# Kernel optimization log

Measured on AMD Instinct MI355X. Metric: run time of the kernel, lower is better.

The kernel has to match this reference:

```python
import jax, jax.numpy as jnp
import numpy as np

B, F, T = 256, 513, 512   # batch, x_dim, seq_len
Z, H, DX, ZG, DZX = 16, 128, 256, 32, 128

def _lin(key, out_d, in_d):
    k1, k2 = jax.random.split(key)
    s = 1.0 / np.sqrt(in_d)
    W = jax.random.uniform(k1, (out_d, in_d), minval=-s, maxval=s, dtype=jnp.float32)
    b = jax.random.uniform(k2, (out_d,), minval=-s, maxval=s, dtype=jnp.float32)
    return W, b

def setup_inputs() -> dict:
    key = jax.random.key(0)
    ks = jax.random.split(key, 20)
    d = {}
    d['x'] = jax.random.normal(ks[0], (B, F, T), dtype=jnp.float32)
    d['eps'] = jax.random.normal(ks[1], (T, B, Z), dtype=jnp.float32)  # reparam noise per step
    # mlp_x_gx: Linear(513,256)+tanh
    d['W_xg'], d['b_xg'] = _lin(ks[2], DX, F)
    # LSTM(256,128), torch gate order i,f,g,o
    s = 1.0 / np.sqrt(H)
    k1, k2, k3, k4 = jax.random.split(ks[3], 4)
    d['W_ih'] = jax.random.uniform(k1, (4 * H, DX), minval=-s, maxval=s, dtype=jnp.float32)
    d['W_hh'] = jax.random.uniform(k2, (4 * H, H), minval=-s, maxval=s, dtype=jnp.float32)
    d['b_ih'] = jax.random.uniform(k3, (4 * H,), minval=-s, maxval=s, dtype=jnp.float32)
    d['b_hh'] = jax.random.uniform(k4, (4 * H,), minval=-s, maxval=s, dtype=jnp.float32)
    # mlp_ztm1_g: Linear(16,32)+tanh, Linear(32,128)+tanh
    d['W_zg0'], d['b_zg0'] = _lin(ks[4], ZG, Z)
    d['W_zg1'], d['b_zg1'] = _lin(ks[5], H, ZG)
    # mlp_g_z = Identity (dense_g_z=[0]); inf heads Linear(128,16)
    d['W_im'], d['b_im'] = _lin(ks[6], Z, H)
    d['W_il'], d['b_il'] = _lin(ks[7], Z, H)
    # gating unit: Linear(16,16)+ReLU, Linear(16,16)+Sigmoid
    d['W_gate0'], d['b_gate0'] = _lin(ks[8], Z, Z)
    d['W_gate1'], d['b_gate1'] = _lin(ks[9], Z, Z)
    # proposed mean: Linear(16,16)+ReLU, Linear(16,16)+Sigmoid
    d['W_prop0'], d['b_prop0'] = _lin(ks[10], Z, Z)
    d['W_prop1'], d['b_prop1'] = _lin(ks[11], Z, Z)
    # prior_mean Linear(16,16); prior_logvar ReLU->Linear(16,16)->Softplus
    d['W_pm'], d['b_pm'] = _lin(ks[12], Z, Z)
    d['W_pl'], d['b_pl'] = _lin(ks[13], Z, Z)
    # mlp_z_x: Linear(16,128)+tanh, Linear(128,128)+tanh; gen_logvar Linear(128,513)
    d['W_zx0'], d['b_zx0'] = _lin(ks[14], DZX, Z)
    d['W_zx1'], d['b_zx1'] = _lin(ks[15], DZX, DZX)
    d['W_gy'], d['b_gy'] = _lin(ks[16], F, DZX)
    return d

def reference(x, eps, W_xg, b_xg, W_ih, W_hh, b_ih, b_hh, W_zg0, b_zg0, W_zg1, b_zg1,
              W_im, b_im, W_il, b_il, W_gate0, b_gate0, W_gate1, b_gate1,
              W_prop0, b_prop0, W_prop1, b_prop1, W_pm, b_pm, W_pl, b_pl,
              W_zx0, b_zx0, W_zx1, b_zx1, W_gy, b_gy):
    xs = jnp.transpose(x, (2, 0, 1))                 # [T,B,F]
    xg = jnp.tanh(xs @ W_xg.T + b_xg)                # [T,B,DX]
    bsz = xs.shape[1]
    Hd = W_hh.shape[1]

    def lstm_step(carry, xt):
        h, c = carry
        gates = xt @ W_ih.T + b_ih + h @ W_hh.T + b_hh
        i, f, g, o = jnp.split(gates, 4, axis=-1)
        c = jax.nn.sigmoid(f) * c + jax.nn.sigmoid(i) * jnp.tanh(g)
        h = jax.nn.sigmoid(o) * jnp.tanh(c)
        return (h, c), h

    h0 = jnp.zeros((bsz, Hd), xg.dtype)
    # module runs LSTM on flipped sequence, then flips output back
    _, g_rev = jax.lax.scan(lstm_step, (h0, h0), xg[::-1])
    g = g_rev[::-1]                                   # [T,B,H]

    def inf_step(z_t, inp):
        g_rnn, e = inp
        hz = jnp.tanh(z_t @ W_zg0.T + b_zg0)
        hz = jnp.tanh(hz @ W_zg1.T + b_zg1)
        g_t = (hz + g_rnn) * 0.5                      # mlp_g_z is Identity
        zm = g_t @ W_im.T + b_im
        zl = g_t @ W_il.T + b_il
        z_new = zm + e * jnp.exp(0.5 * zl)            # reparameterization
        return z_new, (z_new, zm, zl)

    z0 = jnp.zeros((bsz, W_im.shape[0]), xg.dtype)
    _, (z, z_mean, z_logvar) = jax.lax.scan(inf_step, z0, (g, eps))

    # generation_z (gated) -- stored as attributes in the torch module
    z_tm1 = jnp.concatenate([z0[None], z[:-1]], axis=0)
    prop = jax.nn.sigmoid(jax.nn.relu(z_tm1 @ W_prop0.T + b_prop0) @ W_prop1.T + b_prop1)
    gate = jax.nn.sigmoid(jax.nn.relu(z_tm1 @ W_gate0.T + b_gate0) @ W_gate1.T + b_gate1)
    z_mean_p = (1.0 - gate) * (z_tm1 @ W_pm.T + b_pm) + gate * prop
    z_logvar_p = jnp.log(jax.nn.softplus(jax.nn.relu(prop) @ W_pl.T + b_pl))

    # generation_x
    hy = jnp.tanh(z @ W_zx0.T + b_zx0)
    hy = jnp.tanh(hy @ W_zx1.T + b_zx1)
    y = jnp.exp(hy @ W_gy.T + b_gy)                   # [T,B,F]
    return jnp.transpose(y, (1, 2, 0))                # [B,F,T] (forward returns self.y)
```

## Files before the change

kernel.cpp:

```cpp
#include <hip/hip_runtime.h>
#include <cstdint>

#define T_DIM 512
#define B_DIM 256
#define F_DIM 513
#define DX    256
#define H_DIM 128
#define G4    512
#define Z_DIM 16
#define ZG_D  32
#define DZX_D 128
#define M_ROWS (B_DIM * T_DIM)

__device__ __forceinline__ float fast_tanh(float x) {
    return 1.0f - 2.0f / (__expf(2.0f * x) + 1.0f);
}
__device__ __forceinline__ float fast_sig(float x) {
    return 1.0f / (1.0f + __expf(-x));
}

__global__ void bias_comb_kernel(const float* __restrict__ a,
                                 const float* __restrict__ b,
                                 float* __restrict__ c) {
    int i = threadIdx.x;
    if (i < G4) c[i] = a[i] + b[i];
}

template<int ACT, int AMODE, int CMODE, bool GUARD>
__global__ __launch_bounds__(256, 3) void gemm_kernel(
    const float* __restrict__ A, const float* __restrict__ W,
    const float* __restrict__ bias, float* __restrict__ C,
    int M, int N, int K)
{
    __shared__ float As[16][136];
    __shared__ float Bs[16][136];
    const int tid = threadIdx.x;
    const int m0 = blockIdx.y * 128;
    const int n0 = blockIdx.x * 128;
    const int tm = tid >> 4;
    const int tn = tid & 15;
    float acc[8][8] = {};
    const int kTiles = (K + 15) >> 4;
    for (int kt = 0; kt < kTiles; ++kt) {
        const int k0 = kt << 4;
        if (AMODE == 0) {
            const int m  = tid >> 1;
            const int kh = tid & 1;
            const float* ap = &A[(size_t)(m0 + m) * K + k0 + kh * 8];
            const float4 v0 = *(const float4*)(ap);
            const float4 v1 = *(const float4*)(ap + 4);
            As[kh * 8 + 0][m] = v0.x; As[kh * 8 + 1][m] = v0.y;
            As[kh * 8 + 2][m] = v0.z; As[kh * 8 + 3][m] = v0.w;
            As[kh * 8 + 4][m] = v1.x; As[kh * 8 + 5][m] = v1.y;
            As[kh * 8 + 6][m] = v1.z; As[kh * 8 + 7][m] = v1.w;
        } else {
            const int m  = tid & 127;
            const int kh = tid >> 7;
            const int mg = m0 + m;
            const int bb = mg >> 9;
            const int tt = mg & 511;
            const size_t base = (size_t)bb * (F_DIM * T_DIM) + tt;
            #pragma unroll
            for (int j = 0; j < 8; ++j) {
                const int k = k0 + kh * 8 + j;
                As[kh * 8 + j][m] = (k < K) ? A[base + (size_t)k * T_DIM] : 0.0f;
            }
        }
        {
            const int n  = tid >> 1;
            const int kh = tid & 1;
            const int ng = n0 + n;
            if (!GUARD) {
                const float* wp = &W[(size_t)ng * K + k0 + kh * 8];
                const float4 v0 = *(const float4*)(wp);
                const float4 v1 = *(const float4*)(wp + 4);
                Bs[kh * 8 + 0][n] = v0.x; Bs[kh * 8 + 1][n] = v0.y;
                Bs[kh * 8 + 2][n] = v0.z; Bs[kh * 8 + 3][n] = v0.w;
                Bs[kh * 8 + 4][n] = v1.x; Bs[kh * 8 + 5][n] = v1.y;
                Bs[kh * 8 + 6][n] = v1.z; Bs[kh * 8 + 7][n] = v1.w;
            } else {
                #pragma unroll
                for (int j = 0; j < 8; ++j) {
                    const int k = k0 + kh * 8 + j;
                    float v = 0.0f;
                    if (ng < N && k < K) v = W[(size_t)ng * K + k];
                    Bs[kh * 8 + j][n] = v;
                }
            }
        }
        __syncthreads();
        #pragma unroll
        for (int kk = 0; kk < 16; ++kk) {
            const float4 a0 = *(const float4*)&As[kk][tm * 4];
            const float4 a1 = *(const float4*)&As[kk][tm * 4 + 64];
            const float4 b0 = *(const float4*)&Bs[kk][tn * 4];
            const float4 b1 = *(const float4*)&Bs[kk][tn * 4 + 64];
            const float a[8] = { a0.x, a0.y, a0.z, a0.w, a1.x, a1.y, a1.z, a1.w };
            const float b[8] = { b0.x, b0.y, b0.z, b0.w, b1.x, b1.y, b1.z, b1.w };
            #pragma unroll
            for (int i = 0; i < 8; ++i)
                #pragma unroll
                for (int j = 0; j < 8; ++j)
                    acc[i][j] += a[i] * b[j];
        }
        __syncthreads();
    }
    #pragma unroll
    for (int i = 0; i < 8; ++i) {
        const int m = m0 + ((i < 4) ? (tm * 4 + i) : (tm * 4 + 64 + (i - 4)));
        if (CMODE == 0) {
            float r0[4], r1[4];
            #pragma unroll
            for (int j = 0; j < 4; ++j) {
                const int na = n0 + tn * 4 + j;
                float v = acc[i][j] + bias[na];
                if (ACT == 1) v = fast_tanh(v);
                else if (ACT == 2) v = __expf(v);
                r0[j] = v;
                const int nb = n0 + 64 + tn * 4 + j;
                float u = acc[i][j + 4] + bias[nb];
                if (ACT == 1) u = fast_tanh(u);
                else if (ACT == 2) u = __expf(u);
                r1[j] = u;
            }
            *(float4*)&C[(size_t)m * N + n0 + tn * 4]      = make_float4(r0[0], r0[1], r0[2], r0[3]);
            *(float4*)&C[(size_t)m * N + n0 + 64 + tn * 4] = make_float4(r1[0], r1[1], r1[2], r1[3]);
        } else {
            const int bb = m >> 9;
            const int tt = m & 511;
            #pragma unroll
            for (int j = 0; j < 8; ++j) {
                const int n = n0 + ((j < 4) ? (tn * 4 + j) : (64 + tn * 4 + (j - 4)));
                if (n < N) {
                    float v = acc[i][j] + bias[n];
                    if (ACT == 1) v = fast_tanh(v);
                    else if (ACT == 2) v = __expf(v);
                    C[(size_t)bb * (F_DIM * T_DIM) + (size_t)n * T_DIM + tt] = v;
                }
            }
        }
    }
}

#define PIN4(v) asm volatile("" : "+v"((v).x), "+v"((v).y), "+v"((v).z), "+v"((v).w))

__global__ __launch_bounds__(512, 2) void lstm_kernel(
    const float* __restrict__ gin,
    const float* __restrict__ W_hh,
    float* __restrict__ g_out)
{
    __shared__ float hbuf[2][128];
    const int tid  = threadIdx.x;
    const int b    = blockIdx.x;
    const int lane = tid & 63;
    const int w    = tid >> 6;
    const int j    = w * 16 + (lane & 15);
    const int kq   = lane >> 4;

    float4 wi[8], wf[8], wg[8], wo[8];
    {
        const float4* w4 = (const float4*)W_hh;
        const int cb = kq * 8;
        #pragma unroll
        for (int q = 0; q < 8; ++q) {
            wi[q] = w4[(size_t)(j      ) * 32 + cb + q];
            wf[q] = w4[(size_t)(j + 128) * 32 + cb + q];
            wg[q] = w4[(size_t)(j + 256) * 32 + cb + q];
            wo[q] = w4[(size_t)(j + 384) * 32 + cb + q];
        }
        #pragma unroll
        for (int q = 0; q < 8; ++q) { PIN4(wi[q]); PIN4(wf[q]); PIN4(wg[q]); PIN4(wo[q]); }
    }
    if (tid < 128) { hbuf[0][tid] = 0.f; hbuf[1][tid] = 0.f; }
    float c = 0.0f;
    __syncthreads();

    const float* ginb = gin + (size_t)b * T_DIM * G4;
    float gi = ginb[(size_t)(T_DIM - 1) * G4 + j];
    float gf = ginb[(size_t)(T_DIM - 1) * G4 + j + 128];
    float gg = ginb[(size_t)(T_DIM - 1) * G4 + j + 256];
    float go = ginb[(size_t)(T_DIM - 1) * G4 + j + 384];

    int buf = 0;
    for (int t = T_DIM - 1; t >= 0; --t) {
        float ngi = 0.f, ngf = 0.f, ngg = 0.f, ngo = 0.f;
        if (t > 0) {
            const size_t base = (size_t)(t - 1) * G4;
            ngi = ginb[base + j];
            ngf = ginb[base + j + 128];
            ngg = ginb[base + j + 256];
            ngo = ginb[base + j + 384];
        }
        float si = 0.f, sf = 0.f, sg = 0.f, so = 0.f;
        {
            const float4* h4 = (const float4*)&hbuf[buf][kq * 32];
            #pragma unroll
            for (int q = 0; q < 8; ++q) {
                const float4 hv = h4[q];
                si += wi[q].x * hv.x + wi[q].y * hv.y + wi[q].z * hv.z + wi[q].w * hv.w;
                sf += wf[q].x * hv.x + wf[q].y * hv.y + wf[q].z * hv.z + wf[q].w * hv.w;
                sg += wg[q].x * hv.x + wg[q].y * hv.y + wg[q].z * hv.z + wg[q].w * hv.w;
                so += wo[q].x * hv.x + wo[q].y * hv.y + wo[q].z * hv.z + wo[q].w * hv.w;
            }
        }
        si += __shfl_xor(si, 16, 64); si += __shfl_xor(si, 32, 64);
        sf += __shfl_xor(sf, 16, 64); sf += __shfl_xor(sf, 32, 64);
        sg += __shfl_xor(sg, 16, 64); sg += __shfl_xor(sg, 32, 64);
        so += __shfl_xor(so, 16, 64); so += __shfl_xor(so, 32, 64);
        si += gi; sf += gf; sg += gg; so += go;
        c = fast_sig(sf) * c + fast_sig(si) * fast_tanh(sg);
        const float h = fast_sig(so) * fast_tanh(c);
        buf ^= 1;
        if (kq == 0) {
            hbuf[buf][j] = h;
            g_out[((size_t)b * T_DIM + t) * H_DIM + j] = h;
        }
        __syncthreads();
        gi = ngi; gf = ngf; gg = ngg; go = ngo;
        #pragma unroll
        for (int q = 0; q < 8; ++q) { PIN4(wi[q]); PIN4(wf[q]); PIN4(wg[q]); PIN4(wo[q]); }
    }
}

__global__ __launch_bounds__(64, 1) void infer_kernel(
    const float* __restrict__ g,
    const float* __restrict__ eps,
    const float* __restrict__ W_zg0, const float* __restrict__ b_zg0,
    const float* __restrict__ W_zg1, const float* __restrict__ b_zg1,
    const float* __restrict__ W_im,  const float* __restrict__ b_im,
    const float* __restrict__ W_il,  const float* __restrict__ b_il,
    float* __restrict__ z_out)
{
    __shared__ float zbuf[16];
    __shared__ float hzbuf[32];
    __shared__ float h2buf[128];
    const int l = threadIdx.x;
    const int b = blockIdx.x;

    const int r0 = l & 31;
    float4 wz0[4];
    #pragma unroll
    for (int q = 0; q < 4; ++q) wz0[q] = ((const float4*)W_zg0)[r0 * 4 + q];
    const float bz0 = b_zg0[r0];
    float4 w1a[8], w1b[8];
    #pragma unroll
    for (int q = 0; q < 8; ++q) {
        w1a[q] = ((const float4*)W_zg1)[l * 8 + q];
        w1b[q] = ((const float4*)W_zg1)[(l + 64) * 8 + q];
    }
    const float bz1a = b_zg1[l], bz1b = b_zg1[l + 64];
    const int o = l & 31;
    const int half = l >> 5;
    const float* w3p = (o < 16) ? (W_im + o * 128) : (W_il + (o - 16) * 128);
    float4 w3[16];
    #pragma unroll
    for (int q = 0; q < 16; ++q) w3[q] = ((const float4*)(w3p + half * 64))[q];
    const float b3 = (o < 16) ? b_im[o] : b_il[o - 16];

    if (l < 16) zbuf[l] = 0.0f;
    __syncthreads();

    const float* gb = g + (size_t)b * T_DIM * 128;
    float ngl0 = gb[l];
    float ngl1 = gb[64 + l];
    float neps = (l < 16) ? eps[(size_t)b * 16 + l] : 0.0f;
    for (int t = 0; t < T_DIM; ++t) {
        const float gl0 = ngl0, gl1 = ngl1, epsv = neps;
        if (t + 1 < T_DIM) {
            ngl0 = gb[(size_t)(t + 1) * 128 + l];
            ngl1 = gb[(size_t)(t + 1) * 128 + 64 + l];
            neps = (l < 16) ? eps[((size_t)(t + 1) * B_DIM + b) * 16 + l] : 0.0f;
        }
        float s1 = bz0;
        {
            const float4* z4 = (const float4*)zbuf;
            #pragma unroll
            for (int q = 0; q < 4; ++q) {
                const float4 zv = z4[q];
                s1 += wz0[q].x * zv.x + wz0[q].y * zv.y + wz0[q].z * zv.z + wz0[q].w * zv.w;
            }
        }
        const float hz = fast_tanh(s1);
        __syncthreads();
        if (l < 32) hzbuf[l] = hz;
        __syncthreads();
        float s2a = bz1a, s2b = bz1b;
        {
            const float4* hz4 = (const float4*)hzbuf;
            #pragma unroll
            for (int q = 0; q < 8; ++q) {
                const float4 hv = hz4[q];
                s2a += w1a[q].x * hv.x + w1a[q].y * hv.y + w1a[q].z * hv.z + w1a[q].w * hv.w;
                s2b += w1b[q].x * hv.x + w1b[q].y * hv.y + w1b[q].z * hv.z + w1b[q].w * hv.w;
            }
        }
        const float gt0 = 0.5f * (fast_tanh(s2a) + gl0);
        const float gt1 = 0.5f * (fast_tanh(s2b) + gl1);
        __syncthreads();
        h2buf[l]      = gt0;
        h2buf[l + 64] = gt1;
        __syncthreads();
        float s3 = 0.0f;
        {
            const float4* h24 = (const float4*)(h2buf + half * 64);
            #pragma unroll
            for (int q = 0; q < 16; ++q) {
                const float4 hv = h24[q];
                s3 += w3[q].x * hv.x + w3[q].y * hv.y + w3[q].z * hv.z + w3[q].w * hv.w;
            }
        }
        const float full = s3 + __shfl_xor(s3, 32, 64);
        const float val = full + b3;
        const float other = __shfl_xor(val, 16, 64);
        const float znew = val + epsv * __expf(0.5f * other);
        __syncthreads();
        if (l < 16) {
            zbuf[l] = znew;
            z_out[((size_t)b * T_DIM + t) * 16 + l] = znew;
        }
        __syncthreads();
    }
}

extern "C" void kernel_launch(void* const* d_in, const int* in_sizes, int n_in,
                              void* d_out, int out_size, void* d_ws, size_t ws_size,
                              hipStream_t stream)
{
    const float* x     = (const float*)d_in[0];
    const float* eps   = (const float*)d_in[1];
    const float* W_xg  = (const float*)d_in[2];
    const float* b_xg  = (const float*)d_in[3];
    const float* W_ih  = (const float*)d_in[4];
    const float* W_hh  = (const float*)d_in[5];
    const float* b_ih  = (const float*)d_in[6];
    const float* b_hh  = (const float*)d_in[7];
    const float* W_zg0 = (const float*)d_in[8];
    const float* b_zg0 = (const float*)d_in[9];
    const float* W_zg1 = (const float*)d_in[10];
    const float* b_zg1 = (const float*)d_in[11];
    const float* W_im  = (const float*)d_in[12];
    const float* b_im  = (const float*)d_in[13];
    const float* W_il  = (const float*)d_in[14];
    const float* b_il  = (const float*)d_in[15];
    const float* W_zx0 = (const float*)d_in[28];
    const float* b_zx0 = (const float*)d_in[29];
    const float* W_zx1 = (const float*)d_in[30];
    const float* b_zx1 = (const float*)d_in[31];
    const float* W_gy  = (const float*)d_in[32];
    const float* b_gy  = (const float*)d_in[33];
    float* out = (float*)d_out;
    float* ws  = (float*)d_ws;

    float* xg  = ws;
    float* gin = ws + 33554432ull;
    float* g   = ws + 100663296ull;
    float* z   = ws + 117440512ull;
    float* bc  = ws + 119537664ull;
    float* hy1 = ws;
    float* hy2 = ws + 16777216ull;

    bias_comb_kernel<<<1, 512, 0, stream>>>(b_ih, b_hh, bc);
    gemm_kernel<1, 1, 0, true><<<dim3(DX / 128, M_ROWS / 128), 256, 0, stream>>>(
        x, W_xg, b_xg, xg, M_ROWS, DX, F_DIM);
    gemm_kernel<0, 0, 0, false><<<dim3(G4 / 128, M_ROWS / 128), 256, 0, stream>>>(
        xg, W_ih, bc, gin, M_ROWS, G4, DX);
    lstm_kernel<<<B_DIM, 512, 0, stream>>>(gin, W_hh, g);
    infer_kernel<<<B_DIM, 64, 0, stream>>>(g, eps, W_zg0, b_zg0, W_zg1, b_zg1,
                                           W_im, b_im, W_il, b_il, z);
    gemm_kernel<1, 0, 0, false><<<dim3(DZX_D / 128, M_ROWS / 128), 256, 0, stream>>>(
        z, W_zx0, b_zx0, hy1, M_ROWS, DZX_D, Z_DIM);
    gemm_kernel<1, 0, 0, false><<<dim3(DZX_D / 128, M_ROWS / 128), 256, 0, stream>>>(
        hy1, W_zx1, b_zx1, hy2, M_ROWS, DZX_D, DZX_D);
    gemm_kernel<2, 0, 1, true><<<dim3(5, M_ROWS / 128), 256, 0, stream>>>(
        hy2, W_gy, b_gy, out, M_ROWS, F_DIM, DZX_D);
}
```

Before: 3.021 ms.

## Double-buffer GEMM shared tiles and stage transposed output through LDS

Adds register-staged double buffering to the generic GEMM, so global loads for the next k-tile are issued before the FMA loop on the current tile and committed to the alternate LDS buffer, leaving one barrier per iteration instead of two. The transposed output path (CMODE 1, used for the final exp output written as [B,F,T]) now goes through shared memory in 16-row chunks and is written as coalesced float4 rows along T, instead of scattered scalar stores. The cost is twice the LDS footprint, which may lower occupancy, plus extra registers for staging and extra barriers in the epilogue.

Measured after the change: 2.988 ms. Within noise of the previous version (-1.1%).

```diff
diff --git a/kernel.cpp b/kernel.cpp
--- a/kernel.cpp
+++ b/kernel.cpp
@@ -26,14 +26,74 @@
     if (i < G4) c[i] = a[i] + b[i];
 }
 
+#define GEMM_STAGE(kt_) do {                                                   \
+    const int k0s_ = (kt_) << 4;                                               \
+    if (AMODE == 0) {                                                          \
+        const float* ap_ = &A[(size_t)(m0 + (tid >> 1)) * K + k0s_ + (tid & 1) * 8]; \
+        const float4 v0_ = *(const float4*)(ap_);                              \
+        const float4 v1_ = *(const float4*)(ap_ + 4);                          \
+        sa0 = v0_.x; sa1 = v0_.y; sa2 = v0_.z; sa3 = v0_.w;                    \
+        sa4 = v1_.x; sa5 = v1_.y; sa6 = v1_.z; sa7 = v1_.w;                    \
+    } else {                                                                   \
+        const int mg_ = m0 + (tid & 127);                                      \
+        const size_t base_ = (size_t)(mg_ >> 9) * (F_DIM * T_DIM) + (mg_ & 511); \
+        const int kb_ = k0s_ + (tid >> 7) * 8;                                 \
+        sa0 = (kb_ + 0 < K) ? A[base_ + (size_t)(kb_ + 0) * T_DIM] : 0.0f;     \
+        sa1 = (kb_ + 1 < K) ? A[base_ + (size_t)(kb_ + 1) * T_DIM] : 0.0f;     \
+        sa2 = (kb_ + 2 < K) ? A[base_ + (size_t)(kb_ + 2) * T_DIM] : 0.0f;     \
+        sa3 = (kb_ + 3 < K) ? A[base_ + (size_t)(kb_ + 3) * T_DIM] : 0.0f;     \
+        sa4 = (kb_ + 4 < K) ? A[base_ + (size_t)(kb_ + 4) * T_DIM] : 0.0f;     \
+        sa5 = (kb_ + 5 < K) ? A[base_ + (size_t)(kb_ + 5) * T_DIM] : 0.0f;     \
+        sa6 = (kb_ + 6 < K) ? A[base_ + (size_t)(kb_ + 6) * T_DIM] : 0.0f;     \
+        sa7 = (kb_ + 7 < K) ? A[base_ + (size_t)(kb_ + 7) * T_DIM] : 0.0f;     \
+    }                                                                          \
+    {                                                                          \
+        const int ng_ = n0 + (tid >> 1);                                       \
+        const int kb_ = k0s_ + (tid & 1) * 8;                                  \
+        if (!GUARD) {                                                          \
+            const float* wp_ = &W[(size_t)ng_ * K + kb_];                      \
+            const float4 v0_ = *(const float4*)(wp_);                          \
+            const float4 v1_ = *(const float4*)(wp_ + 4);                      \
+            sb0 = v0_.x; sb1 = v0_.y; sb2 = v0_.z; sb3 = v0_.w;                \
+            sb4 = v1_.x; sb5 = v1_.y; sb6 = v1_.z; sb7 = v1_.w;                \
+        } else {                                                               \
+            const size_t wb_ = (size_t)ng_ * K;                                \
+            const bool okn_ = (ng_ < N);                                       \
+            sb0 = (okn_ && kb_ + 0 < K) ? W[wb_ + kb_ + 0] : 0.0f;             \
+            sb1 = (okn_ && kb_ + 1 < K) ? W[wb_ + kb_ + 1] : 0.0f;             \
+            sb2 = (okn_ && kb_ + 2 < K) ? W[wb_ + kb_ + 2] : 0.0f;             \
+            sb3 = (okn_ && kb_ + 3 < K) ? W[wb_ + kb_ + 3] : 0.0f;             \
+            sb4 = (okn_ && kb_ + 4 < K) ? W[wb_ + kb_ + 4] : 0.0f;             \
+            sb5 = (okn_ && kb_ + 5 < K) ? W[wb_ + kb_ + 5] : 0.0f;             \
+            sb6 = (okn_ && kb_ + 6 < K) ? W[wb_ + kb_ + 6] : 0.0f;             \
+            sb7 = (okn_ && kb_ + 7 < K) ? W[wb_ + kb_ + 7] : 0.0f;             \
+        }                                                                      \
+    }                                                                          \
+} while (0)
+
+#define GEMM_COMMIT(bi_) do {                                                  \
+    const int ma_ = (AMODE == 0) ? (tid >> 1) : (tid & 127);                   \
+    const int ka_ = ((AMODE == 0) ? (tid & 1) : (tid >> 7)) * 8;               \
+    As[bi_][ka_ + 0][ma_] = sa0; As[bi_][ka_ + 1][ma_] = sa1;                  \
+    As[bi_][ka_ + 2][ma_] = sa2; As[bi_][ka_ + 3][ma_] = sa3;                  \
+    As[bi_][ka_ + 4][ma_] = sa4; As[bi_][ka_ + 5][ma_] = sa5;                  \
+    As[bi_][ka_ + 6][ma_] = sa6; As[bi_][ka_ + 7][ma_] = sa7;                  \
+    const int nb_ = tid >> 1;                                                  \
+    const int kc_ = (tid & 1) * 8;                                             \
+    Bs[bi_][kc_ + 0][nb_] = sb0; Bs[bi_][kc_ + 1][nb_] = sb1;                  \
+    Bs[bi_][kc_ + 2][nb_] = sb2; Bs[bi_][kc_ + 3][nb_] = sb3;                  \
+    Bs[bi_][kc_ + 4][nb_] = sb4; Bs[bi_][kc_ + 5][nb_] = sb5;                  \
+    Bs[bi_][kc_ + 6][nb_] = sb6; Bs[bi_][kc_ + 7][nb_] = sb7;                  \
+} while (0)
+
 template<int ACT, int AMODE, int CMODE, bool GUARD>
 __global__ __launch_bounds__(256, 3) void gemm_kernel(
     const float* __restrict__ A, const float* __restrict__ W,
     const float* __restrict__ bias, float* __restrict__ C,
     int M, int N, int K)
 {
-    __shared__ float As[16][136];
-    __shared__ float Bs[16][136];
+    __shared__ float As[2][16][136];
+    __shared__ float Bs[2][16][136];
     const int tid = threadIdx.x;
     const int m0 = blockIdx.y * 128;
     const int n0 = blockIdx.x * 128;
@@ -41,60 +101,23 @@
     const int tn = tid & 15;
     float acc[8][8] = {};
     const int kTiles = (K + 15) >> 4;
+
+    float sa0, sa1, sa2, sa3, sa4, sa5, sa6, sa7;
+    float sb0, sb1, sb2, sb3, sb4, sb5, sb6, sb7;
+
+    GEMM_STAGE(0);
+    GEMM_COMMIT(0);
+    __syncthreads();
+    int cur = 0;
     for (int kt = 0; kt < kTiles; ++kt) {
-        const int k0 = kt << 4;
-        if (AMODE == 0) {
-            const int m  = tid >> 1;
-            const int kh = tid & 1;
-            const float* ap = &A[(size_t)(m0 + m) * K + k0 + kh * 8];
-            const float4 v0 = *(const float4*)(ap);
-            const float4 v1 = *(const float4*)(ap + 4);
-            As[kh * 8 + 0][m] = v0.x; As[kh * 8 + 1][m] = v0.y;
-            As[kh * 8 + 2][m] = v0.z; As[kh * 8 + 3][m] = v0.w;
-            As[kh * 8 + 4][m] = v1.x; As[kh * 8 + 5][m] = v1.y;
-            As[kh * 8 + 6][m] = v1.z; As[kh * 8 + 7][m] = v1.w;
-        } else {
-            const int m  = tid & 127;
-            const int kh = tid >> 7;
-            const int mg = m0 + m;
-            const int bb = mg >> 9;
-            const int tt = mg & 511;
-            const size_t base = (size_t)bb * (F_DIM * T_DIM) + tt;
-            #pragma unroll
-            for (int j = 0; j < 8; ++j) {
-                const int k = k0 + kh * 8 + j;
-                As[kh * 8 + j][m] = (k < K) ? A[base + (size_t)k * T_DIM] : 0.0f;
-            }
-        }
-        {
-            const int n  = tid >> 1;
-            const int kh = tid & 1;
-            const int ng = n0 + n;
-            if (!GUARD) {
-                const float* wp = &W[(size_t)ng * K + k0 + kh * 8];
-                const float4 v0 = *(const float4*)(wp);
-                const float4 v1 = *(const float4*)(wp + 4);
-                Bs[kh * 8 + 0][n] = v0.x; Bs[kh * 8 + 1][n] = v0.y;
-                Bs[kh * 8 + 2][n] = v0.z; Bs[kh * 8 + 3][n] = v0.w;
-                Bs[kh * 8 + 4][n] = v1.x; Bs[kh * 8 + 5][n] = v1.y;
-                Bs[kh * 8 + 6][n] = v1.z; Bs[kh * 8 + 7][n] = v1.w;
-            } else {
-                #pragma unroll
-                for (int j = 0; j < 8; ++j) {
-                    const int k = k0 + kh * 8 + j;
-                    float v = 0.0f;
-                    if (ng < N && k < K) v = W[(size_t)ng * K + k];
-                    Bs[kh * 8 + j][n] = v;
-                }
-            }
-        }
-        __syncthreads();
+        const int ktn = (kt + 1 < kTiles) ? (kt + 1) : kt;
+        GEMM_STAGE(ktn);
         #pragma unroll
         for (int kk = 0; kk < 16; ++kk) {
-            const float4 a0 = *(const float4*)&As[kk][tm * 4];
-            const float4 a1 = *(const float4*)&As[kk][tm * 4 + 64];
-            const float4 b0 = *(const float4*)&Bs[kk][tn * 4];
-            const float4 b1 = *(const float4*)&Bs[kk][tn * 4 + 64];
+            const float4 a0 = *(const float4*)&As[cur][kk][tm * 4];
+            const float4 a1 = *(const float4*)&As[cur][kk][tm * 4 + 64];
+            const float4 b0 = *(const float4*)&Bs[cur][kk][tn * 4];
+            const float4 b1 = *(const float4*)&Bs[cur][kk][tn * 4 + 64];
             const float a[8] = { a0.x, a0.y, a0.z, a0.w, a1.x, a1.y, a1.z, a1.w };
             const float b[8] = { b0.x, b0.y, b0.z, b0.w, b1.x, b1.y, b1.z, b1.w };
             #pragma unroll
@@ -103,12 +126,14 @@
                 for (int j = 0; j < 8; ++j)
                     acc[i][j] += a[i] * b[j];
         }
-        __syncthreads();
-    }
-    #pragma unroll
-    for (int i = 0; i < 8; ++i) {
-        const int m = m0 + ((i < 4) ? (tm * 4 + i) : (tm * 4 + 64 + (i - 4)));
-        if (CMODE == 0) {
+        GEMM_COMMIT(cur ^ 1);
+        __syncthreads();
+        cur ^= 1;
+    }
+    if (CMODE == 0) {
+        #pragma unroll
+        for (int i = 0; i < 8; ++i) {
+            const int m = m0 + ((i < 4) ? (tm * 4 + i) : (tm * 4 + 64 + (i - 4)));
             float r0[4], r1[4];
             #pragma unroll
             for (int j = 0; j < 4; ++j) {
@@ -125,17 +150,40 @@
             }
             *(float4*)&C[(size_t)m * N + n0 + tn * 4]      = make_float4(r0[0], r0[1], r0[2], r0[3]);
             *(float4*)&C[(size_t)m * N + n0 + 64 + tn * 4] = make_float4(r1[0], r1[1], r1[2], r1[3]);
-        } else {
-            const int bb = m >> 9;
-            const int tt = m & 511;
+        }
+    } else {
+        const int bb  = m0 >> 9;
+        const int tt0 = m0 & 511;
+        float* Cb = C + (size_t)bb * (F_DIM * T_DIM) + tt0;
+        #pragma unroll
+        for (int chunk = 0; chunk < 8; ++chunk) {
+            __syncthreads();
             #pragma unroll
             for (int j = 0; j < 8; ++j) {
-                const int n = n0 + ((j < 4) ? (tn * 4 + j) : (64 + tn * 4 + (j - 4)));
+                const int ln = (j < 4) ? (tn * 4 + j) : (64 + tn * 4 + (j - 4));
+                if ((ln >> 4) == chunk) {
+                    const int n = n0 + ln;
+                    if (n < N) {
+                        const float bn = bias[n];
+                        #pragma unroll
+                        for (int i = 0; i < 8; ++i) {
+                            const int lm = (i < 4) ? (tm * 4 + i) : (64 + tm * 4 + (i - 4));
+                            float v = acc[i][j] + bn;
+                            if (ACT == 1) v = fast_tanh(v);
+                            else if (ACT == 2) v = __expf(v);
+                            As[0][ln & 15][lm] = v;
+                        }
+                    }
+                }
+            }
+            __syncthreads();
+            #pragma unroll
+            for (int p = 0; p < 2; ++p) {
+                const int r = (tid >> 5) + p * 8;
+                const int c = (tid & 31) * 4;
+                const int n = n0 + chunk * 16 + r;
                 if (n < N) {
-                    float v = acc[i][j] + bias[n];
-                    if (ACT == 1) v = fast_tanh(v);
-                    else if (ACT == 2) v = __expf(v);
-                    C[(size_t)bb * (F_DIM * T_DIM) + (size_t)n * T_DIM + tt] = v;
+                    *(float4*)&Cb[(size_t)n * T_DIM + c] = *(const float4*)&As[0][r][c];
                 }
             }
         }
```
